# Performance work log

Measured on AMD Instinct MI355X. Metric: run time of the kernel, lower is better.

The kernel has to match this reference:

```python
import jax, jax.numpy as jnp
import numpy as np

XD = 256      # x_dim
NI = 128      # n_ineq
ND = XD + NI  # n_dim (primal + slack)
PD = XD + NI  # parm_dim
B = 256
STEPS = 5
ALPHA = 0.5
GAMMA = 1.0 / (2.0 * 1.0)  # module does gamma <- 1/(2*gamma), gamma0=1.0
UPPER = 1000.0


def setup_inputs() -> dict:
    key = jax.random.key(0)
    k1, k2, k3, k4 = jax.random.split(key, 4)
    x = jax.random.normal(k1, (B, XD), dtype=jnp.float32)
    parms = jax.random.normal(k2, (B, PD), dtype=jnp.float32)
    M = jax.random.normal(k3, (XD, XD), dtype=jnp.float32)
    Q = M @ M.T / XD + jnp.eye(XD, dtype=jnp.float32)  # PSD Hessian of f_obj
    A = jax.random.normal(k4, (NI, XD), dtype=jnp.float32) / np.float32(np.sqrt(XD))
    return {"x": x, "parms": parms, "Q": Q, "A": A}


def _foF(z, p, Q, A):
    """SecondOrderObjectiveConstraintComposition, one sample.
    Solves min_d g.d + 0.5 d'Hd + GAMMA d'P d  s.t.  F(z) + J d = 0  (P = I metric),
    i.e. one regularized SQP/prox step on xs = [x; s] with F(xs)=F_ineq(x)+s (pid=2)."""
    fobj = lambda xs: 0.5 * xs[:XD] @ (Q @ xs[:XD]) + p[:XD] @ xs[:XD]
    Ffun = lambda xs: A @ xs[:XD] - p[XD:ND] + xs[XD:]
    g = jax.grad(fobj)(z)                 # (ND,)
    H = jax.hessian(fobj)(z)              # (ND, ND)
    J = jax.jacfwd(Ffun)(z)               # (NI, ND)
    Fz = Ffun(z)                          # (NI,)
    KKT = jnp.block([[H + 2.0 * GAMMA * jnp.eye(ND, dtype=z.dtype), J.T],
                     [J, jnp.zeros((NI, NI), dtype=z.dtype)]])
    rhs = jnp.concatenate([-g, -Fz])
    sol = jnp.linalg.solve(KKT, rhs)
    return z + sol[:ND]


def _forward(x, parms, Q, A):
    lower = jnp.concatenate([-UPPER * jnp.ones(XD, x.dtype), jnp.zeros(NI, x.dtype)])
    xs0 = jnp.concatenate([x, jnp.zeros((x.shape[0], NI), x.dtype)], axis=-1)  # slack append
    w0 = jnp.zeros_like(xs0)
    step = jax.vmap(_foF, in_axes=(0, 0, None, None))

    def body(carry, _):
        y, w = carry
        xk = step(y - w, parms, Q, A)
        xA = 2.0 * ALPHA * xk + (1.0 - 2.0 * ALPHA) * y
        y_new = jnp.clip(xA + w, lower, UPPER)      # BoxConstraint projection
        w_new = w + xA - y_new                       # dual update
        return (y_new, w_new), (xk, xk - y_new, y_new - y)

    _, (xks, rgaps, sgaps) = jax.lax.scan(body, (xs0, w0), None, length=STEPS)
    x_hist = jnp.concatenate([xs0[None], xks], axis=0)  # (STEPS+1, B, ND)
    x_out = xks[-1][:, :XD]                             # drop slacks
    return x_out, rgaps[-1], sgaps[-1], x_hist


def reference(x, parms, Q, A):
    return _forward(x, parms, Q, A)
```

## Files before the change

kernel.cpp:

```cpp
#include <hip/hip_runtime.h>

#define XD 256
#define NI 128
#define ND 384
#define BATCH 256
#define NSTEPS 5
#define NS_ITERS 7

#define K_OFF   0
#define X0_OFF  (65536)
#define X1_OFF  (65536*2)
#define T_OFF   (65536*3)
#define U_OFF   (65536*4)
#define ZA_OFF  (65536*4 + 147456)
#define ZB_OFF  (ZA_OFF + BATCH*ND)
#define W_OFF   (ZB_OFF + BATCH*ND)
#define SC_OFF  (W_OFF + BATCH*ND)

template<bool BT>
__global__ __launch_bounds__(256)
void gemm_kernel(const float* __restrict__ A, int lda,
                 const float* __restrict__ B, int ldb,
                 float* __restrict__ C, int ldc,
                 int M, int N, int K, float scale,
                 const float* __restrict__ Cadd, int ldca, float caddScale)
{
    __shared__ float As[32][33];
    __shared__ float Bs[32][33];
    const int tx = threadIdx.x, ty = threadIdx.y;
    const int tid = ty * 16 + tx;
    const int n0 = blockIdx.x * 32, m0 = blockIdx.y * 32;
    float acc00 = 0.f, acc01 = 0.f, acc10 = 0.f, acc11 = 0.f;

    for (int k0 = 0; k0 < K; k0 += 32) {
#pragma unroll
        for (int it = 0; it < 4; ++it) {
            int idx = tid + it * 256;
            int mm = idx >> 5, kk = idx & 31;
            As[mm][kk] = A[(m0 + mm) * lda + (k0 + kk)];
        }
#pragma unroll
        for (int it = 0; it < 4; ++it) {
            int idx = tid + it * 256;
            if (BT) {
                int nn = idx >> 5, kk = idx & 31;
                Bs[kk][nn] = B[(n0 + nn) * ldb + (k0 + kk)];
            } else {
                int kk = idx >> 5, nn = idx & 31;
                Bs[kk][nn] = B[(k0 + kk) * ldb + (n0 + nn)];
            }
        }
        __syncthreads();
#pragma unroll
        for (int kk = 0; kk < 32; ++kk) {
            float a0 = As[2 * ty][kk], a1 = As[2 * ty + 1][kk];
            float b0 = Bs[kk][2 * tx], b1 = Bs[kk][2 * tx + 1];
            acc00 += a0 * b0; acc01 += a0 * b1;
            acc10 += a1 * b0; acc11 += a1 * b1;
        }
        __syncthreads();
    }

    float accs[2][2] = {{acc00, acc01}, {acc10, acc11}};
#pragma unroll
    for (int i = 0; i < 2; ++i)
#pragma unroll
        for (int j = 0; j < 2; ++j) {
            int m = m0 + 2 * ty + i, n = n0 + 2 * tx + j;
            float v = scale * accs[i][j];
            if (Cadd) v += caddScale * Cadd[m * ldca + n];
            C[m * ldc + n] = v;
        }
}

__global__ __launch_bounds__(256)
void build_K_kernel(const float* __restrict__ A, const float* __restrict__ Q,
                    float* __restrict__ Kout)
{
    __shared__ float Ai[32][33];
    __shared__ float Aj[32][33];
    const int tx = threadIdx.x, ty = threadIdx.y;
    const int tid = ty * 16 + tx;
    const int n0 = blockIdx.x * 32, m0 = blockIdx.y * 32;
    float acc00 = 0.f, acc01 = 0.f, acc10 = 0.f, acc11 = 0.f;

    for (int k0 = 0; k0 < NI; k0 += 32) {
#pragma unroll
        for (int it = 0; it < 4; ++it) {
            int idx = tid + it * 256;
            int kk = idx >> 5, col = idx & 31;
            Ai[kk][col] = A[(k0 + kk) * XD + (m0 + col)];
            Aj[kk][col] = A[(k0 + kk) * XD + (n0 + col)];
        }
        __syncthreads();
#pragma unroll
        for (int kk = 0; kk < 32; ++kk) {
            float a0 = Ai[kk][2 * ty], a1 = Ai[kk][2 * ty + 1];
            float b0 = Aj[kk][2 * tx], b1 = Aj[kk][2 * tx + 1];
            acc00 += a0 * b0; acc01 += a0 * b1;
            acc10 += a1 * b0; acc11 += a1 * b1;
        }
        __syncthreads();
    }

    float accs[2][2] = {{acc00, acc01}, {acc10, acc11}};
#pragma unroll
    for (int i = 0; i < 2; ++i)
#pragma unroll
        for (int j = 0; j < 2; ++j) {
            int m = m0 + 2 * ty + i, n = n0 + 2 * tx + j;
            float v = accs[i][j] + Q[m * XD + n];
            if (m == n) v += 1.0f;
            Kout[m * XD + n] = v;
        }
}

__global__ __launch_bounds__(256)
void rowmax_kernel(const float* __restrict__ K, float* __restrict__ sc)
{
    const int t = threadIdx.x;
    float s = 0.f;
    for (int j = 0; j < XD; ++j) s += fabsf(K[j * XD + t]);
    __shared__ float red[256];
    red[t] = s;
    __syncthreads();
    for (int off = 128; off; off >>= 1) {
        if (t < off) red[t] = fmaxf(red[t], red[t + off]);
        __syncthreads();
    }
    if (t == 0) sc[0] = 2.0f / (2.0f + red[0]);
}

__global__ __launch_bounds__(256)
void ns_init_kernel(const float* __restrict__ K, const float* __restrict__ sc,
                    float* __restrict__ X)
{
    int idx = blockIdx.x * 256 + threadIdx.x;
    float c = sc[0];
    int i = idx >> 8, j = idx & 255;
    float v = -c * c * K[idx];
    if (i == j) v += 2.0f * c;
    X[idx] = v;
}

__global__ __launch_bounds__(256)
void copyXU_kernel(const float* __restrict__ X, float* __restrict__ U)
{
    int idx = blockIdx.x * 256 + threadIdx.x;
    int i = idx >> 8, j = idx & 255;
    U[i * ND + j] = X[idx];
}

__global__ __launch_bounds__(256)
void init_state_kernel(const float* __restrict__ x, float* __restrict__ z,
                       float* __restrict__ w, float* __restrict__ xh0)
{
    int idx = blockIdx.x * 256 + threadIdx.x;
    int b = idx / ND, i = idx % ND;
    float v = (i < XD) ? x[b * XD + i] : 0.0f;
    z[idx] = v;
    w[idx] = 0.0f;
    xh0[idx] = v;
}

template<bool LAST>
__global__ __launch_bounds__(256)
void step_kernel(const float* __restrict__ zin, float* __restrict__ zout,
                 float* __restrict__ w, const float* __restrict__ p,
                 const float* __restrict__ U,
                 float* __restrict__ xhist,
                 float* __restrict__ xout, float* __restrict__ rgap,
                 float* __restrict__ sgap)
{
    __shared__ float Es[32][33];
    __shared__ float Us[32][33];
    const int tx = threadIdx.x, ty = threadIdx.y;
    const int tid = ty * 16 + tx;
    const int n0 = blockIdx.x * 32, m0 = blockIdx.y * 32;
    float acc00 = 0.f, acc01 = 0.f, acc10 = 0.f, acc11 = 0.f;

    for (int k0 = 0; k0 < ND; k0 += 32) {
#pragma unroll
        for (int it = 0; it < 4; ++it) {
            int idx = tid + it * 256;
            int mm = idx >> 5, kk = idx & 31;
            int g = (m0 + mm) * ND + (k0 + kk);
            Es[mm][kk] = zin[g] - p[g];
        }
#pragma unroll
        for (int it = 0; it < 4; ++it) {
            int idx = tid + it * 256;
            int nn = idx >> 5, kk = idx & 31;
            Us[kk][nn] = U[(n0 + nn) * ND + (k0 + kk)];
        }
        __syncthreads();
#pragma unroll
        for (int kk = 0; kk < 32; ++kk) {
            float a0 = Es[2 * ty][kk], a1 = Es[2 * ty + 1][kk];
            float b0 = Us[kk][2 * tx], b1 = Us[kk][2 * tx + 1];
            acc00 += a0 * b0; acc01 += a0 * b1;
            acc10 += a1 * b0; acc11 += a1 * b1;
        }
        __syncthreads();
    }

    float accs[2][2] = {{acc00, acc01}, {acc10, acc11}};
#pragma unroll
    for (int i = 0; i < 2; ++i)
#pragma unroll
        for (int j = 0; j < 2; ++j) {
            int m = m0 + 2 * ty + i, n = n0 + 2 * tx + j;
            int g = m * ND + n;
            float xk = accs[i][j] + ((n >= XD) ? p[g] : 0.0f);
            float zv = zin[g];
            float wv = w[g];
            float v = xk + wv;
            float lo = (n < XD) ? -1000.0f : 0.0f;
            float ynew = fminf(fmaxf(v, lo), 1000.0f);
            float wnew = v - ynew;
            xhist[g] = xk;
            zout[g] = 2.0f * ynew - v;
            w[g] = wnew;
            if (LAST) {
                rgap[g] = xk - ynew;
                sgap[g] = ynew - (zv + wv);
                if (n < XD) xout[m * XD + n] = xk;
            }
        }
}

extern "C" void kernel_launch(void* const* d_in, const int* in_sizes, int n_in,
                              void* d_out, int out_size, void* d_ws, size_t ws_size,
                              hipStream_t stream)
{
    const float* x = (const float*)d_in[0];
    const float* p = (const float*)d_in[1];
    const float* Q = (const float*)d_in[2];
    const float* A = (const float*)d_in[3];

    float* ws = (float*)d_ws;
    float* Kw   = ws + K_OFF;
    float* Xbuf[2] = { ws + X0_OFF, ws + X1_OFF };
    float* T    = ws + T_OFF;
    float* U    = ws + U_OFF;
    float* Z[2] = { ws + ZA_OFF, ws + ZB_OFF };
    float* W    = ws + W_OFF;
    float* sc   = ws + SC_OFF;

    float* out   = (float*)d_out;
    float* xout  = out;
    float* rgap  = out + BATCH * XD;
    float* sgap  = rgap + BATCH * ND;
    float* xhist = sgap + BATCH * ND;

    dim3 blk(16, 16);

    build_K_kernel<<<dim3(8, 8), blk, 0, stream>>>(A, Q, Kw);
    rowmax_kernel<<<1, 256, 0, stream>>>(Kw, sc);
    ns_init_kernel<<<256, 256, 0, stream>>>(Kw, sc, Xbuf[0]);

    int cur = 0;
    for (int it = 0; it < NS_ITERS; ++it) {
        gemm_kernel<false><<<dim3(8, 8), blk, 0, stream>>>(
            Kw, XD, Xbuf[cur], XD, T, XD, XD, XD, XD, 1.0f, nullptr, 0, 0.0f);
        gemm_kernel<false><<<dim3(8, 8), blk, 0, stream>>>(
            Xbuf[cur], XD, T, XD, Xbuf[cur ^ 1], XD, XD, XD, XD, -1.0f,
            Xbuf[cur], XD, 2.0f);
        cur ^= 1;
    }

    copyXU_kernel<<<256, 256, 0, stream>>>(Xbuf[cur], U);
    gemm_kernel<true><<<dim3(4, 8), blk, 0, stream>>>(
        Xbuf[cur], XD, A, XD, U + XD, ND, XD, NI, XD, -1.0f, nullptr, 0, 0.0f);
    gemm_kernel<false><<<dim3(12, 4), blk, 0, stream>>>(
        A, XD, U, ND, U + XD * ND, ND, NI, ND, XD, -1.0f, nullptr, 0, 0.0f);

    init_state_kernel<<<384, 256, 0, stream>>>(x, Z[0], W, xhist);

    for (int s = 0; s < NSTEPS; ++s) {
        float* zin = Z[s & 1];
        float* zout_ = Z[(s & 1) ^ 1];
        float* xh = xhist + (size_t)(s + 1) * BATCH * ND;
        if (s == NSTEPS - 1)
            step_kernel<true><<<dim3(12, 8), blk, 0, stream>>>(
                zin, zout_, W, p, U, xh, xout, rgap, sgap);
        else
            step_kernel<false><<<dim3(12, 8), blk, 0, stream>>>(
                zin, zout_, W, p, U, xh, xout, rgap, sgap);
    }
}
```

Before: 320.0 us.

## Fuse entire pipeline into one cooperative kernel with grid syncs

Replaces about 25 separate kernel launches with a single cooperative kernel of 128 blocks that steps through the phases separated by grid.sync(). It also recasts the Newton-Schulz inverse iteration as coupled Y/X updates (Y=I-cK style), so the two GEMMs of each iteration run concurrently on different blocks. Small independent work such as state init and the U copy is moved onto otherwise idle blocks. The intent is to remove launch overhead and serialization between tiny GEMMs, at the cost of grid-wide barriers and only 128 blocks of parallelism.

```diff
diff --git a/kernel.cpp b/kernel.cpp
--- a/kernel.cpp
+++ b/kernel.cpp
@@ -1,291 +1,270 @@
 #include <hip/hip_runtime.h>
+#include <hip/hip_cooperative_groups.h>
+
+namespace cg = cooperative_groups;
 
 #define XD 256
 #define NI 128
 #define ND 384
 #define BATCH 256
-#define NSTEPS 5
-#define NS_ITERS 7
-
-#define K_OFF   0
-#define X0_OFF  (65536)
-#define X1_OFF  (65536*2)
-#define T_OFF   (65536*3)
-#define U_OFF   (65536*4)
-#define ZA_OFF  (65536*4 + 147456)
-#define ZB_OFF  (ZA_OFF + BATCH*ND)
-#define W_OFF   (ZB_OFF + BATCH*ND)
-#define SC_OFF  (W_OFF + BATCH*ND)
-
-template<bool BT>
-__global__ __launch_bounds__(256)
-void gemm_kernel(const float* __restrict__ A, int lda,
-                 const float* __restrict__ B, int ldb,
-                 float* __restrict__ C, int ldc,
-                 int M, int N, int K, float scale,
-                 const float* __restrict__ Cadd, int ldca, float caddScale)
+#define NFUSED 6
+
+template<int AMODE, int BMODE>
+__device__ __forceinline__ void gemm32(
+    const float* __restrict__ Ag, const float* __restrict__ A2, int lda,
+    const float* __restrict__ Bg, int ldb,
+    int m0, int n0, int Kdim,
+    float* __restrict__ As, float* __restrict__ Bs,
+    int tid, int tx, int ty, float acc[2][2])
 {
-    __shared__ float As[32][33];
-    __shared__ float Bs[32][33];
-    const int tx = threadIdx.x, ty = threadIdx.y;
-    const int tid = ty * 16 + tx;
-    const int n0 = blockIdx.x * 32, m0 = blockIdx.y * 32;
-    float acc00 = 0.f, acc01 = 0.f, acc10 = 0.f, acc11 = 0.f;
-
-    for (int k0 = 0; k0 < K; k0 += 32) {
+    for (int k0 = 0; k0 < Kdim; k0 += 32) {
 #pragma unroll
         for (int it = 0; it < 4; ++it) {
             int idx = tid + it * 256;
-            int mm = idx >> 5, kk = idx & 31;
-            As[mm][kk] = A[(m0 + mm) * lda + (k0 + kk)];
+            int mm, kk;
+            if (AMODE == 1) { mm = idx & 31; kk = idx >> 5; }
+            else           { mm = idx >> 5; kk = idx & 31; }
+            float v;
+            if (AMODE == 1) v = Ag[(k0 + kk) * lda + (m0 + mm)];
+            else            v = Ag[(m0 + mm) * lda + (k0 + kk)];
+            if (AMODE == 2) v -= A2[(m0 + mm) * lda + (k0 + kk)];
+            As[kk * 34 + mm] = v;
         }
 #pragma unroll
         for (int it = 0; it < 4; ++it) {
             int idx = tid + it * 256;
-            if (BT) {
+            if (BMODE == 1) {
                 int nn = idx >> 5, kk = idx & 31;
-                Bs[kk][nn] = B[(n0 + nn) * ldb + (k0 + kk)];
+                Bs[kk * 34 + nn] = Bg[(n0 + nn) * ldb + (k0 + kk)];
             } else {
                 int kk = idx >> 5, nn = idx & 31;
-                Bs[kk][nn] = B[(k0 + kk) * ldb + (n0 + nn)];
+                float v = Bg[(k0 + kk) * ldb + (n0 + nn)];
+                if (BMODE == 2) v = ((k0 + kk) == (n0 + nn)) ? 2.0f - v : -v;
+                Bs[kk * 34 + nn] = v;
             }
         }
         __syncthreads();
 #pragma unroll
         for (int kk = 0; kk < 32; ++kk) {
-            float a0 = As[2 * ty][kk], a1 = As[2 * ty + 1][kk];
-            float b0 = Bs[kk][2 * tx], b1 = Bs[kk][2 * tx + 1];
-            acc00 += a0 * b0; acc01 += a0 * b1;
-            acc10 += a1 * b0; acc11 += a1 * b1;
+            float2 a = *(const float2*)(As + kk * 34 + 2 * ty);
+            float2 b = *(const float2*)(Bs + kk * 34 + 2 * tx);
+            acc[0][0] = fmaf(a.x, b.x, acc[0][0]);
+            acc[0][1] = fmaf(a.x, b.y, acc[0][1]);
+            acc[1][0] = fmaf(a.y, b.x, acc[1][0]);
+            acc[1][1] = fmaf(a.y, b.y, acc[1][1]);
         }
         __syncthreads();
     }
-
-    float accs[2][2] = {{acc00, acc01}, {acc10, acc11}};
-#pragma unroll
-    for (int i = 0; i < 2; ++i)
-#pragma unroll
-        for (int j = 0; j < 2; ++j) {
-            int m = m0 + 2 * ty + i, n = n0 + 2 * tx + j;
-            float v = scale * accs[i][j];
-            if (Cadd) v += caddScale * Cadd[m * ldca + n];
-            C[m * ldc + n] = v;
-        }
 }
 
-__global__ __launch_bounds__(256)
-void build_K_kernel(const float* __restrict__ A, const float* __restrict__ Q,
-                    float* __restrict__ Kout)
+__global__ void __launch_bounds__(256)
+admm_all(const float* __restrict__ x, const float* __restrict__ parms,
+         const float* __restrict__ Q, const float* __restrict__ A,
+         float* __restrict__ ws, float* __restrict__ out)
 {
-    __shared__ float Ai[32][33];
-    __shared__ float Aj[32][33];
-    const int tx = threadIdx.x, ty = threadIdx.y;
-    const int tid = ty * 16 + tx;
-    const int n0 = blockIdx.x * 32, m0 = blockIdx.y * 32;
-    float acc00 = 0.f, acc01 = 0.f, acc10 = 0.f, acc11 = 0.f;
-
-    for (int k0 = 0; k0 < NI; k0 += 32) {
-#pragma unroll
-        for (int it = 0; it < 4; ++it) {
-            int idx = tid + it * 256;
-            int kk = idx >> 5, col = idx & 31;
-            Ai[kk][col] = A[(k0 + kk) * XD + (m0 + col)];
-            Aj[kk][col] = A[(k0 + kk) * XD + (n0 + col)];
-        }
+    cg::grid_group grid = cg::this_grid();
+    __shared__ float As[32 * 34];
+    __shared__ float Bs[32 * 34];
+    __shared__ float red[256];
+    const int tid = threadIdx.x;
+    const int tx = tid & 15, ty = tid >> 4;
+    const int bid = blockIdx.x;
+
+    float* Kw   = ws;
+    float* Yb[2] = { ws + 65536, ws + 131072 };
+    float* Xb[2] = { ws + 196608, ws + 262144 };
+    float* U    = ws + 327680;
+    float* Z[2] = { ws + 475136, ws + 573440 };
+    float* W    = ws + 671744;
+    float* sc   = ws + 770048;
+
+    float* xout  = out;
+    float* rgap  = out + BATCH * XD;
+    float* sgap  = rgap + BATCH * ND;
+    float* xhist = sgap + BATCH * ND;
+
+    if (bid < 64) {
+        int m0 = (bid >> 3) * 32, n0 = (bid & 7) * 32;
+        float acc[2][2] = {};
+        gemm32<1, 0>(A, nullptr, XD, A, XD, m0, n0, NI, As, Bs, tid, tx, ty, acc);
+#pragma unroll
+        for (int i = 0; i < 2; ++i)
+#pragma unroll
+            for (int j = 0; j < 2; ++j) {
+                int m = m0 + 2 * ty + i, n = n0 + 2 * tx + j;
+                Kw[m * XD + n] = acc[i][j] + Q[m * XD + n] + (m == n ? 1.0f : 0.0f);
+            }
+    } else {
+        int base = (bid - 64) * 256 + tid;
+#pragma unroll
+        for (int r = 0; r < 6; ++r) {
+            int e = base + r * 16384;
+            int b = e / ND, i2 = e % ND;
+            float v = (i2 < XD) ? x[b * XD + i2] : 0.0f;
+            Z[0][e] = v;
+            W[e] = 0.0f;
+            xhist[e] = v;
+        }
+    }
+    grid.sync();
+
+    if (bid == 0) {
+        float s = 0.f;
+        for (int j = 0; j < XD; ++j) s += fabsf(Kw[j * XD + tid]);
+        red[tid] = s;
         __syncthreads();
-#pragma unroll
-        for (int kk = 0; kk < 32; ++kk) {
-            float a0 = Ai[kk][2 * ty], a1 = Ai[kk][2 * ty + 1];
-            float b0 = Aj[kk][2 * tx], b1 = Aj[kk][2 * tx + 1];
-            acc00 += a0 * b0; acc01 += a0 * b1;
-            acc10 += a1 * b0; acc11 += a1 * b1;
-        }
-        __syncthreads();
-    }
-
-    float accs[2][2] = {{acc00, acc01}, {acc10, acc11}};
-#pragma unroll
-    for (int i = 0; i < 2; ++i)
-#pragma unroll
-        for (int j = 0; j < 2; ++j) {
-            int m = m0 + 2 * ty + i, n = n0 + 2 * tx + j;
-            float v = accs[i][j] + Q[m * XD + n];
-            if (m == n) v += 1.0f;
-            Kout[m * XD + n] = v;
-        }
-}
-
-__global__ __launch_bounds__(256)
-void rowmax_kernel(const float* __restrict__ K, float* __restrict__ sc)
-{
-    const int t = threadIdx.x;
-    float s = 0.f;
-    for (int j = 0; j < XD; ++j) s += fabsf(K[j * XD + t]);
-    __shared__ float red[256];
-    red[t] = s;
-    __syncthreads();
-    for (int off = 128; off; off >>= 1) {
-        if (t < off) red[t] = fmaxf(red[t], red[t + off]);
-        __syncthreads();
-    }
-    if (t == 0) sc[0] = 2.0f / (2.0f + red[0]);
-}
-
-__global__ __launch_bounds__(256)
-void ns_init_kernel(const float* __restrict__ K, const float* __restrict__ sc,
-                    float* __restrict__ X)
-{
-    int idx = blockIdx.x * 256 + threadIdx.x;
-    float c = sc[0];
-    int i = idx >> 8, j = idx & 255;
-    float v = -c * c * K[idx];
-    if (i == j) v += 2.0f * c;
-    X[idx] = v;
-}
-
-__global__ __launch_bounds__(256)
-void copyXU_kernel(const float* __restrict__ X, float* __restrict__ U)
-{
-    int idx = blockIdx.x * 256 + threadIdx.x;
-    int i = idx >> 8, j = idx & 255;
-    U[i * ND + j] = X[idx];
-}
-
-__global__ __launch_bounds__(256)
-void init_state_kernel(const float* __restrict__ x, float* __restrict__ z,
-                       float* __restrict__ w, float* __restrict__ xh0)
-{
-    int idx = blockIdx.x * 256 + threadIdx.x;
-    int b = idx / ND, i = idx % ND;
-    float v = (i < XD) ? x[b * XD + i] : 0.0f;
-    z[idx] = v;
-    w[idx] = 0.0f;
-    xh0[idx] = v;
-}
-
-template<bool LAST>
-__global__ __launch_bounds__(256)
-void step_kernel(const float* __restrict__ zin, float* __restrict__ zout,
-                 float* __restrict__ w, const float* __restrict__ p,
-                 const float* __restrict__ U,
-                 float* __restrict__ xhist,
-                 float* __restrict__ xout, float* __restrict__ rgap,
-                 float* __restrict__ sgap)
-{
-    __shared__ float Es[32][33];
-    __shared__ float Us[32][33];
-    const int tx = threadIdx.x, ty = threadIdx.y;
-    const int tid = ty * 16 + tx;
-    const int n0 = blockIdx.x * 32, m0 = blockIdx.y * 32;
-    float acc00 = 0.f, acc01 = 0.f, acc10 = 0.f, acc11 = 0.f;
-
-    for (int k0 = 0; k0 < ND; k0 += 32) {
-#pragma unroll
-        for (int it = 0; it < 4; ++it) {
-            int idx = tid + it * 256;
-            int mm = idx >> 5, kk = idx & 31;
-            int g = (m0 + mm) * ND + (k0 + kk);
-            Es[mm][kk] = zin[g] - p[g];
-        }
-#pragma unroll
-        for (int it = 0; it < 4; ++it) {
-            int idx = tid + it * 256;
-            int nn = idx >> 5, kk = idx & 31;
-            Us[kk][nn] = U[(n0 + nn) * ND + (k0 + kk)];
-        }
-        __syncthreads();
-#pragma unroll
-        for (int kk = 0; kk < 32; ++kk) {
-            float a0 = Es[2 * ty][kk], a1 = Es[2 * ty + 1][kk];
-            float b0 = Us[kk][2 * tx], b1 = Us[kk][2 * tx + 1];
-            acc00 += a0 * b0; acc01 += a0 * b1;
-            acc10 += a1 * b0; acc11 += a1 * b1;
-        }
-        __syncthreads();
-    }
-
-    float accs[2][2] = {{acc00, acc01}, {acc10, acc11}};
-#pragma unroll
-    for (int i = 0; i < 2; ++i)
-#pragma unroll
-        for (int j = 0; j < 2; ++j) {
-            int m = m0 + 2 * ty + i, n = n0 + 2 * tx + j;
-            int g = m * ND + n;
-            float xk = accs[i][j] + ((n >= XD) ? p[g] : 0.0f);
-            float zv = zin[g];
-            float wv = w[g];
-            float v = xk + wv;
-            float lo = (n < XD) ? -1000.0f : 0.0f;
-            float ynew = fminf(fmaxf(v, lo), 1000.0f);
-            float wnew = v - ynew;
-            xhist[g] = xk;
-            zout[g] = 2.0f * ynew - v;
-            w[g] = wnew;
-            if (LAST) {
-                rgap[g] = xk - ynew;
-                sgap[g] = ynew - (zv + wv);
-                if (n < XD) xout[m * XD + n] = xk;
+        for (int off = 128; off; off >>= 1) {
+            if (tid < off) red[tid] = fmaxf(red[tid], red[tid + off]);
+            __syncthreads();
+        }
+        if (tid == 0) sc[0] = 2.0f / (2.0f + red[0]);
+    }
+    grid.sync();
+
+    const float c = sc[0];
+
+    if (bid < 64) {
+        int m0 = (bid >> 3) * 32, n0 = (bid & 7) * 32;
+        float acc[2][2] = {};
+        gemm32<0, 0>(Kw, nullptr, XD, Kw, XD, m0, n0, XD, As, Bs, tid, tx, ty, acc);
+#pragma unroll
+        for (int i = 0; i < 2; ++i)
+#pragma unroll
+            for (int j = 0; j < 2; ++j) {
+                int m = m0 + 2 * ty + i, n = n0 + 2 * tx + j;
+                int g = m * XD + n;
+                Yb[0][g] = 2.0f * c * Kw[g] - c * c * acc[i][j];
             }
-        }
+    } else {
+        int base = (bid - 64) * 256 + tid;
+#pragma unroll
+        for (int r = 0; r < 4; ++r) {
+            int e = base + r * 16384;
+            int i2 = e >> 8, j2 = e & 255;
+            float v = -c * c * Kw[e];
+            if (i2 == j2) v += 2.0f * c;
+            Xb[0][e] = v;
+        }
+    }
+    grid.sync();
+
+    int cur = 0;
+    for (int it2 = 0; it2 < NFUSED; ++it2) {
+        int nxt = cur ^ 1;
+        if (bid < 64) {
+            int m0 = (bid >> 3) * 32, n0 = (bid & 7) * 32;
+            float acc[2][2] = {};
+            gemm32<0, 2>(Yb[cur], nullptr, XD, Yb[cur], XD, m0, n0, XD, As, Bs, tid, tx, ty, acc);
+#pragma unroll
+            for (int i = 0; i < 2; ++i)
+#pragma unroll
+                for (int j = 0; j < 2; ++j)
+                    Yb[nxt][(m0 + 2 * ty + i) * XD + (n0 + 2 * tx + j)] = acc[i][j];
+        } else {
+            int t = bid - 64;
+            int m0 = (t >> 3) * 32, n0 = (t & 7) * 32;
+            float acc[2][2] = {};
+            gemm32<0, 2>(Xb[cur], nullptr, XD, Yb[cur], XD, m0, n0, XD, As, Bs, tid, tx, ty, acc);
+#pragma unroll
+            for (int i = 0; i < 2; ++i)
+#pragma unroll
+                for (int j = 0; j < 2; ++j)
+                    Xb[nxt][(m0 + 2 * ty + i) * XD + (n0 + 2 * tx + j)] = acc[i][j];
+        }
+        cur = nxt;
+        grid.sync();
+    }
+    const float* Xf = Xb[cur];
+
+    if (bid < 32) {
+        int m0 = (bid >> 2) * 32, n0 = (bid & 3) * 32;
+        float acc[2][2] = {};
+        gemm32<0, 1>(Xf, nullptr, XD, A, XD, m0, n0, XD, As, Bs, tid, tx, ty, acc);
+#pragma unroll
+        for (int i = 0; i < 2; ++i)
+#pragma unroll
+            for (int j = 0; j < 2; ++j)
+                U[(m0 + 2 * ty + i) * ND + XD + (n0 + 2 * tx + j)] = -acc[i][j];
+    } else if (bid < 64) {
+        int t = bid - 32;
+        int m0 = (t >> 3) * 32, n0 = (t & 7) * 32;
+        float acc[2][2] = {};
+        gemm32<0, 0>(A, nullptr, XD, Xf, XD, m0, n0, XD, As, Bs, tid, tx, ty, acc);
+#pragma unroll
+        for (int i = 0; i < 2; ++i)
+#pragma unroll
+            for (int j = 0; j < 2; ++j)
+                U[(XD + m0 + 2 * ty + i) * ND + (n0 + 2 * tx + j)] = -acc[i][j];
+    } else {
+        int base = (bid - 64) * 256 + tid;
+#pragma unroll
+        for (int r = 0; r < 4; ++r) {
+            int e = base + r * 16384;
+            int i2 = e >> 8, j2 = e & 255;
+            U[i2 * ND + j2] = Xf[e];
+        }
+    }
+    grid.sync();
+
+    if (bid < 16) {
+        int m0 = (bid >> 2) * 32, n0 = (bid & 3) * 32;
+        float acc[2][2] = {};
+        gemm32<0, 1>(U + XD * ND, nullptr, ND, A, XD, m0, n0, XD, As, Bs, tid, tx, ty, acc);
+#pragma unroll
+        for (int i = 0; i < 2; ++i)
+#pragma unroll
+            for (int j = 0; j < 2; ++j)
+                U[(XD + m0 + 2 * ty + i) * ND + XD + (n0 + 2 * tx + j)] = -acc[i][j];
+    }
+    grid.sync();
+
+    for (int s = 0; s < 5; ++s) {
+        const float* zin = Z[s & 1];
+        float* zo = Z[(s & 1) ^ 1];
+        float* xh = xhist + (size_t)(s + 1) * BATCH * ND;
+        if (bid < 96) {
+            int m0 = (bid / 12) * 32, n0 = (bid % 12) * 32;
+            float acc[2][2] = {};
+            gemm32<2, 1>(zin, parms, ND, U, ND, m0, n0, ND, As, Bs, tid, tx, ty, acc);
+#pragma unroll
+            for (int i = 0; i < 2; ++i)
+#pragma unroll
+                for (int j = 0; j < 2; ++j) {
+                    int m = m0 + 2 * ty + i, n = n0 + 2 * tx + j;
+                    int g = m * ND + n;
+                    float xk = acc[i][j] + ((n >= XD) ? parms[g] : 0.0f);
+                    float zv = zin[g];
+                    float wv = W[g];
+                    float v = xk + wv;
+                    float lo = (n < XD) ? -1000.0f : 0.0f;
+                    float ynew = fminf(fmaxf(v, lo), 1000.0f);
+                    xh[g] = xk;
+                    zo[g] = 2.0f * ynew - v;
+                    W[g] = v - ynew;
+                    if (s == 4) {
+                        rgap[g] = xk - ynew;
+                        sgap[g] = ynew - (zv + wv);
+                        if (n < XD) xout[m * XD + n] = xk;
+                    }
+                }
+        }
+        if (s < 4) grid.sync();
+    }
 }
 
 extern "C" void kernel_launch(void* const* d_in, const int* in_sizes, int n_in,
                               void* d_out, int out_size, void* d_ws, size_t ws_size,
                               hipStream_t stream)
 {
-    const float* x = (const float*)d_in[0];
-    const float* p = (const float*)d_in[1];
-    const float* Q = (const float*)d_in[2];
-    const float* A = (const float*)d_in[3];
-
-    float* ws = (float*)d_ws;
-    float* Kw   = ws + K_OFF;
-    float* Xbuf[2] = { ws + X0_OFF, ws + X1_OFF };
-    float* T    = ws + T_OFF;
-    float* U    = ws + U_OFF;
-    float* Z[2] = { ws + ZA_OFF, ws + ZB_OFF };
-    float* W    = ws + W_OFF;
-    float* sc   = ws + SC_OFF;
-
-    float* out   = (float*)d_out;
-    float* xout  = out;
-    float* rgap  = out + BATCH * XD;
-    float* sgap  = rgap + BATCH * ND;
-    float* xhist = sgap + BATCH * ND;
-
-    dim3 blk(16, 16);
-
-    build_K_kernel<<<dim3(8, 8), blk, 0, stream>>>(A, Q, Kw);
-    rowmax_kernel<<<1, 256, 0, stream>>>(Kw, sc);
-    ns_init_kernel<<<256, 256, 0, stream>>>(Kw, sc, Xbuf[0]);
-
-    int cur = 0;
-    for (int it = 0; it < NS_ITERS; ++it) {
-        gemm_kernel<false><<<dim3(8, 8), blk, 0, stream>>>(
-            Kw, XD, Xbuf[cur], XD, T, XD, XD, XD, XD, 1.0f, nullptr, 0, 0.0f);
-        gemm_kernel<false><<<dim3(8, 8), blk, 0, stream>>>(
-            Xbuf[cur], XD, T, XD, Xbuf[cur ^ 1], XD, XD, XD, XD, -1.0f,
-            Xbuf[cur], XD, 2.0f);
-        cur ^= 1;
-    }
-
-    copyXU_kernel<<<256, 256, 0, stream>>>(Xbuf[cur], U);
-    gemm_kernel<true><<<dim3(4, 8), blk, 0, stream>>>(
-        Xbuf[cur], XD, A, XD, U + XD, ND, XD, NI, XD, -1.0f, nullptr, 0, 0.0f);
-    gemm_kernel<false><<<dim3(12, 4), blk, 0, stream>>>(
-        A, XD, U, ND, U + XD * ND, ND, NI, ND, XD, -1.0f, nullptr, 0, 0.0f);
-
-    init_state_kernel<<<384, 256, 0, stream>>>(x, Z[0], W, xhist);
-
-    for (int s = 0; s < NSTEPS; ++s) {
-        float* zin = Z[s & 1];
-        float* zout_ = Z[(s & 1) ^ 1];
-        float* xh = xhist + (size_t)(s + 1) * BATCH * ND;
-        if (s == NSTEPS - 1)
-            step_kernel<true><<<dim3(12, 8), blk, 0, stream>>>(
-                zin, zout_, W, p, U, xh, xout, rgap, sgap);
-        else
-            step_kernel<false><<<dim3(12, 8), blk, 0, stream>>>(
-                zin, zout_, W, p, U, xh, xout, rgap, sgap);
-    }
+    const float* x     = (const float*)d_in[0];
+    const float* parms = (const float*)d_in[1];
+    const float* Q     = (const float*)d_in[2];
+    const float* A     = (const float*)d_in[3];
+    float* ws  = (float*)d_ws;
+    float* out = (float*)d_out;
+
+    void* args[] = { (void*)&x, (void*)&parms, (void*)&Q, (void*)&A,
+                     (void*)&ws, (void*)&out };
+    hipLaunchCooperativeKernel((const void*)admm_all, dim3(128), dim3(256),
+                               args, 0, stream);
 }
```

After: 588.2 us. +83.8%, slower.
